# Performance work log

Measured on AMD Instinct MI355X. Metric: run time of the kernel, lower is better.

Reference implementation:

```python
import jax, jax.numpy as jnp
import numpy as np

N, M, E, F, OUT = 20000, 2048, 320000, 512, 2
HID = F // 2
NEG_ATT = 0.2   # leaky_relu slope inside HypergraphConv attention
NEG = 0.01      # default F.leaky_relu / nn.LeakyReLU slope
EPS = 1e-5      # GraphNorm eps


def setup_inputs() -> dict:
    key = jax.random.key(0)
    ks = jax.random.split(key, 12)
    nrm = lambda k, shape, s=0.05: (jax.random.normal(k, shape, jnp.float32) * s)
    row = jax.random.randint(ks[1], (E,), 0, N)
    col = jax.random.randint(ks[2], (E,), 0, M)
    return dict(
        x=nrm(ks[0], (N, F), 1.0),
        edge_index=jnp.stack([row, col]),                 # [2, E] int32
        edge_attr=nrm(ks[3], (M, F), 1.0),
        W1=nrm(ks[4], (F, F)), att1=nrm(ks[5], (2 * F,)), b1=jnp.zeros((F,), jnp.float32),
        W2=nrm(ks[6], (F, F)), att2=nrm(ks[7], (2 * F,)), b2=jnp.zeros((F,), jnp.float32),
        gn1_w=jnp.ones((F,), jnp.float32), gn1_b=jnp.zeros((F,), jnp.float32), gn1_ms=jnp.ones((F,), jnp.float32),
        gn2_w=jnp.ones((F,), jnp.float32), gn2_b=jnp.zeros((F,), jnp.float32), gn2_ms=jnp.ones((F,), jnp.float32),
        fc1_W=nrm(ks[8], (F, HID)), fc1_b=jnp.zeros((HID,), jnp.float32),
        fc2_W=nrm(ks[9], (F, HID)), fc2_b=jnp.zeros((HID,), jnp.float32),
        cls_W=nrm(ks[10], (HID, OUT)), cls_b=jnp.zeros((OUT,), jnp.float32),
    )


def _segsum(v, idx, n):
    return jax.ops.segment_sum(v, idx, num_segments=n)


def hypergraph_conv(x, edge_attr, row, col, W, att, bias):
    """PyG HypergraphConv, heads=1, use_attention=True, attention_mode='node'."""
    xl = x @ W                          # [N, F] node features after lin
    el = edge_attr @ W                  # [M, F] hyperedge features after lin
    # attention logits per incidence: (cat[x_i, e_j] * att).sum(-1)
    pre = xl[row] @ att[:F] + el[col] @ att[F:]           # [E]
    alpha = jax.nn.leaky_relu(pre, NEG_ATT)
    # softmax grouped by hyperedge (col)
    amax = jax.ops.segment_max(alpha, col, num_segments=M)
    amax = jnp.where(jnp.isfinite(amax), amax, 0.0)
    ex = jnp.exp(alpha - amax[col])
    denom = _segsum(ex, col, M)
    alpha = ex / jnp.maximum(denom, 1e-16)[col]           # [E]
    # degree normalizations (hyperedge_weight = 1)
    ones = jnp.ones((row.shape[0],), xl.dtype)
    deg_n = _segsum(ones, row, N)
    Dinv = jnp.where(deg_n > 0, 1.0 / deg_n, 0.0)         # [N]
    deg_e = _segsum(ones, col, M)
    Binv = jnp.where(deg_e > 0, 1.0 / deg_e, 0.0)         # [M]
    # propagate 1: nodes -> hyperedges
    edge_feat = _segsum((alpha * Binv[col])[:, None] * xl[row], col, M)   # [M, F]
    # propagate 2: hyperedges -> nodes
    out = _segsum((alpha * Dinv[row])[:, None] * edge_feat[col], row, N)  # [N, F]
    return out + bias


def graph_norm(x, w, b, ms):
    # single graph (batch=None): normalize over all nodes
    mean = x.mean(axis=0)
    out = x - ms * mean
    var = (out * out).mean(axis=0)
    return out / jnp.sqrt(var + EPS) * w + b


def reference(x, edge_index, edge_attr,
              W1, att1, b1, W2, att2, b2,
              gn1_w, gn1_b, gn1_ms, gn2_w, gn2_b, gn2_ms,
              fc1_W, fc1_b, fc2_W, fc2_b, cls_W, cls_b):
    row, col = edge_index[0], edge_index[1]
    h = hypergraph_conv(x, edge_attr, row, col, W1, att1, b1)
    h = jax.nn.leaky_relu(graph_norm(h, gn1_w, gn1_b, gn1_ms), NEG)
    out = jax.nn.leaky_relu(h @ fc1_W + fc1_b, NEG)
    h = hypergraph_conv(h, edge_attr, row, col, W2, att2, b2)
    h = jax.nn.leaky_relu(graph_norm(h, gn2_w, gn2_b, gn2_ms), NEG)
    out = out + jax.nn.leaky_relu(h @ fc2_W + fc2_b, NEG)
    logits = out @ cls_W + cls_b
    return logits
```

## Files before the change

kernel.cpp:

```cpp
#include <hip/hip_runtime.h>
#include <math.h>

#define FDIM 512
#define HIDDIM 256
#define HB 128
#define SCH 1024
#define LDSK 32

typedef __bf16 bf16x8 __attribute__((ext_vector_type(8)));
typedef float floatx4 __attribute__((ext_vector_type(4)));

__device__ __forceinline__ float lrelu(float x, float s) { return x >= 0.0f ? x : s * x; }

__device__ __forceinline__ float bf2f(unsigned int u) {
  union { float f; unsigned int i; } v; v.i = u << 16; return v.f;
}
__device__ __forceinline__ unsigned short f2bf(float f) {
  union { float f; unsigned int u; } v; v.f = f;
  unsigned int x = v.u;
  return (unsigned short)((x + 0x7fffu + ((x >> 16) & 1u)) >> 16);
}

__device__ __forceinline__ void async_copy16(const unsigned short* g, unsigned short* l) {
  __builtin_amdgcn_global_load_lds((const __attribute__((address_space(1))) unsigned int*)g,
                                   (__attribute__((address_space(3))) unsigned int*)l, 16, 0, 0);
}

__device__ __forceinline__ float waveReduceSum(float v) {
#pragma unroll
  for (int o = 32; o; o >>= 1) v += __shfl_down(v, o, 64);
  return v;
}

__device__ __forceinline__ float blockReduceSum256(float v) {
  __shared__ float sm[4];
  int lane = threadIdx.x & 63, w = threadIdx.x >> 6;
  v = waveReduceSum(v);
  __syncthreads();
  if (lane == 0) sm[w] = v;
  __syncthreads();
  return sm[0] + sm[1] + sm[2] + sm[3];
}

__device__ __forceinline__ float blockReduceMax256(float v) {
  __shared__ float sm[4];
  int lane = threadIdx.x & 63, w = threadIdx.x >> 6;
#pragma unroll
  for (int o = 32; o; o >>= 1) v = fmaxf(v, __shfl_down(v, o, 64));
  __syncthreads();
  if (lane == 0) sm[w] = v;
  __syncthreads();
  return fmaxf(fmaxf(sm[0], sm[1]), fmaxf(sm[2], sm[3]));
}

__global__ __launch_bounds__(256) void k_hist2(const int* __restrict__ row, const int* __restrict__ col,
                                               int* __restrict__ cnt_r, int* __restrict__ cnt_c,
                                               int E, int nchunk) {
  __shared__ int h[2048];
  int b = blockIdx.x, t = threadIdx.x;
  for (int i = t; i < 2048; i += 256) h[i] = 0;
  __syncthreads();
  int s = b * nchunk, e = min(E, s + nchunk);
  for (int j = s + t; j < e; j += 256) {
    atomicAdd(&h[col[j]], 1);
    atomicAdd(&cnt_r[row[j]], 1);
  }
  __syncthreads();
  for (int i = t; i < 2048; i += 256) {
    int v = h[i];
    if (v) atomicAdd(&cnt_c[i], v);
  }
}

__global__ __launch_bounds__(256) void k_scan_part(const int* __restrict__ cnt, int* __restrict__ off,
                                                   int* __restrict__ btot, int n) {
  int b = blockIdx.x, t = threadIdx.x;
  int base = b * SCH + t * 4;
  int v[4];
#pragma unroll
  for (int i = 0; i < 4; ++i) v[i] = (base + i < n) ? cnt[base + i] : 0;
  int s = v[0] + v[1] + v[2] + v[3];
  int lane = t & 63, w = t >> 6;
  int x = s;
#pragma unroll
  for (int o = 1; o < 64; o <<= 1) {
    int y = __shfl_up(x, o, 64);
    if (lane >= o) x += y;
  }
  __shared__ int ws[4];
  if (lane == 63) ws[w] = x;
  __syncthreads();
  int wpre = 0;
  for (int i = 0; i < w; ++i) wpre += ws[i];
  int run = wpre + x - s;
#pragma unroll
  for (int i = 0; i < 4; ++i) {
    if (base + i < n) off[base + i] = run;
    run += v[i];
  }
  if (t == 255) btot[b] = wpre + x;
}

__global__ __launch_bounds__(256) void k_scan_mid(int* __restrict__ btot, int nb) {
  int t = threadIdx.x;
  int v = (t < nb) ? btot[t] : 0;
  int lane = t & 63, w = t >> 6;
  int x = v;
#pragma unroll
  for (int o = 1; o < 64; o <<= 1) {
    int y = __shfl_up(x, o, 64);
    if (lane >= o) x += y;
  }
  __shared__ int ws[4];
  if (lane == 63) ws[w] = x;
  __syncthreads();
  int wpre = 0;
  for (int i = 0; i < w; ++i) wpre += ws[i];
  if (t < nb) btot[t] = wpre + x - v;
  if (t == 255) btot[nb] = wpre + x;
}

__global__ __launch_bounds__(256) void k_scan_add(int* __restrict__ off, const int* __restrict__ btot,
                                                  int n, int nb) {
  int b = blockIdx.x, t = threadIdx.x;
  int base = b * SCH + t * 4;
  int add = btot[b];
#pragma unroll
  for (int i = 0; i < 4; ++i)
    if (base + i < n) off[base + i] += add;
  if (b == 0 && t == 0) off[n] = btot[nb];
}

__global__ __launch_bounds__(256) void k_scan2048(const int* __restrict__ cnt, int* __restrict__ off,
                                                  int* __restrict__ gcur) {
  int t = threadIdx.x;
  int base = t * 8;
  int v[8];
#pragma unroll
  for (int i = 0; i < 8; ++i) v[i] = cnt[base + i];
  int s = 0;
#pragma unroll
  for (int i = 0; i < 8; ++i) s += v[i];
  int lane = t & 63, w = t >> 6;
  int x = s;
#pragma unroll
  for (int o = 1; o < 64; o <<= 1) {
    int y = __shfl_up(x, o, 64);
    if (lane >= o) x += y;
  }
  __shared__ int ws[4];
  if (lane == 63) ws[w] = x;
  __syncthreads();
  int wpre = 0;
  for (int i = 0; i < w; ++i) wpre += ws[i];
  int run = wpre + x - s;
#pragma unroll
  for (int i = 0; i < 8; ++i) {
    off[base + i] = run;
    gcur[base + i] = run;
    run += v[i];
  }
  if (t == 255) off[2048] = wpre + x;
}

__global__ __launch_bounds__(256) void k_fill3(const int* __restrict__ row, const int* __restrict__ col,
                                               int* __restrict__ gcur, const int* __restrict__ off_r,
                                               int* __restrict__ cur_r, int* __restrict__ csr_c,
                                               int* __restrict__ rj, int* __restrict__ cj,
                                               int* __restrict__ pos_r, int E, int nchunk) {
  __shared__ int h[2048];
  __shared__ int lbase[2048];
  int b = blockIdx.x, t = threadIdx.x;
  for (int i = t; i < 2048; i += 256) h[i] = 0;
  __syncthreads();
  int s = b * nchunk, e = min(E, s + nchunk);
  for (int j = s + t; j < e; j += 256) atomicAdd(&h[col[j]], 1);
  __syncthreads();
  for (int i = t; i < 2048; i += 256) {
    int c = h[i];
    lbase[i] = c ? atomicAdd(&gcur[i], c) : 0;
    h[i] = 0;
  }
  __syncthreads();
  for (int j = s + t; j < e; j += 256) {
    int r = row[j], c = col[j];
    int slot_c = lbase[c] + atomicAdd(&h[c], 1);
    csr_c[slot_c] = j;
    rj[slot_c] = r;
    int slot_r = off_r[r] + atomicAdd(&cur_r[r], 1);
    cj[slot_r] = c;
    pos_r[j] = slot_r;
  }
}

__global__ __launch_bounds__(256) void k_hi(const float* __restrict__ A, unsigned short* __restrict__ hi, int n4) {
  int i = blockIdx.x * 256 + threadIdx.x;
  if (i < n4) {
    float4 v = ((const float4*)A)[i];
    ushort4 h;
    h.x = f2bf(v.x); h.y = f2bf(v.y); h.z = f2bf(v.z); h.w = f2bf(v.w);
    ((ushort4*)hi)[i] = h;
  }
}

__global__ __launch_bounds__(256) void k_prep_w_hi(const float* __restrict__ W, unsigned short* __restrict__ th,
                                                   int K, int Nc) {
  int n = blockIdx.x * 16 + (threadIdx.x & 15);
  int k = blockIdx.y * 16 + (threadIdx.x >> 4);
  th[(size_t)n * K + k] = f2bf(W[(size_t)k * Nc + n]);
}

__global__ __launch_bounds__(256) void k_prep_w(const float* __restrict__ W, unsigned short* __restrict__ th,
                                                unsigned short* __restrict__ tl, int K, int Nc) {
  int n = blockIdx.x * 16 + (threadIdx.x & 15);
  int k = blockIdx.y * 16 + (threadIdx.x >> 4);
  float v = W[(size_t)k * Nc + n];
  unsigned short h = f2bf(v);
  unsigned short l = f2bf(v - bf2f(h));
  th[(size_t)n * K + k] = h;
  tl[(size_t)n * K + k] = l;
}

__global__ __launch_bounds__(256) void k_wv(const float* __restrict__ W, const float* __restrict__ att,
                                            float* __restrict__ wv) {
  int lane = threadIdx.x & 63, w = threadIdx.x >> 6;
  int k = blockIdx.x * 4 + w;
  float s = 0.f;
  for (int f = lane; f < FDIM; f += 64) s = fmaf(W[(size_t)k * FDIM + f], att[f], s);
  s = waveReduceSum(s);
  if (lane == 0) wv[k] = s;
}

__global__ __launch_bounds__(256) void k_ea(const float* __restrict__ X, const float* __restrict__ wv,
                                            float* __restrict__ out, int Mr) {
  int lane = threadIdx.x & 63, w = threadIdx.x >> 6;
  int m = blockIdx.x * 4 + w;
  if (m < Mr) {
    float s = 0.f;
    for (int f = lane; f < FDIM; f += 64) s = fmaf(X[(size_t)m * FDIM + f], wv[f], s);
    s = waveReduceSum(s);
    if (lane == 0) out[m] = s;
  }
}

__global__ __launch_bounds__(256, 1) void gemm_conv(const unsigned short* __restrict__ Ah,
                                                    const unsigned short* __restrict__ Bth,
                                                    unsigned short* __restrict__ Cb,
                                                    const float* __restrict__ att, float* __restrict__ xa,
                                                    int Mr, int K, int Nc) {
  __shared__ unsigned short lds[2 * 128 * LDSK];
  int tid = threadIdx.x, lane = tid & 63, w = tid >> 6;
  int wr = w >> 1, wc = w & 1;
  int rowB = blockIdx.y * 128, colB = blockIdx.x * 128;

  const unsigned short* src = (w < 2) ? Ah : Bth;
  int baseRow = ((w < 2) ? rowB : colB) + 64 * (w & 1);
  int maxRow = (w < 2) ? (Mr - 1) : (Nc - 1);
  int slr = lane >> 2, slc = lane & 3;
  unsigned short* dstBase = &lds[((w >> 1) * 128 + (w & 1) * 64) * LDSK];

  size_t gro[4];
#pragma unroll
  for (int seg = 0; seg < 4; ++seg) {
    int rg = baseRow + seg * 16 + slr;
    if (rg > maxRow) rg = maxRow;
    gro[seg] = (size_t)rg * K + slc * 8;
  }

  floatx4 zero4 = {0.f, 0.f, 0.f, 0.f};
  floatx4 acc[4][4];
#pragma unroll
  for (int i = 0; i < 4; ++i)
#pragma unroll
    for (int j = 0; j < 4; ++j) acc[i][j] = zero4;

  int fr = lane & 15, fq = lane >> 4;
  int offA = (wr * 64 + fr) * LDSK + fq * 8;
  int offB = 128 * LDSK + (wc * 64 + fr) * LDSK + fq * 8;

  for (int k0 = 0; k0 < K; k0 += 32) {
#pragma unroll
    for (int seg = 0; seg < 4; ++seg) async_copy16(src + gro[seg] + k0, dstBase + seg * 16 * LDSK);
    __syncthreads();
    bf16x8 a[4], b[4];
#pragma unroll
    for (int t = 0; t < 4; ++t) {
      a[t] = *(const bf16x8*)(&lds[offA + t * 16 * LDSK]);
      b[t] = *(const bf16x8*)(&lds[offB + t * 16 * LDSK]);
    }
#pragma unroll
    for (int ti = 0; ti < 4; ++ti)
#pragma unroll
      for (int tj = 0; tj < 4; ++tj)
        acc[ti][tj] = __builtin_amdgcn_mfma_f32_16x16x32_bf16(a[ti], b[tj], acc[ti][tj], 0, 0, 0);
    __syncthreads();
  }

  int colL = colB + wc * 64 + fr;
  int rowL = rowB + wr * 64 + fq * 4;
  float attv[4];
#pragma unroll
  for (int tj = 0; tj < 4; ++tj) attv[tj] = att[colL + tj * 16];
#pragma unroll
  for (int ti = 0; ti < 4; ++ti) {
#pragma unroll
    for (int r = 0; r < 4; ++r) {
      int rr = rowL + ti * 16 + r;
      if (rr < Mr) {
        float dot = 0.f;
#pragma unroll
        for (int tj = 0; tj < 4; ++tj) {
          float v = acc[ti][tj][r];
          Cb[(size_t)rr * Nc + colL + tj * 16] = f2bf(v);
          dot = fmaf(v, attv[tj], dot);
        }
#pragma unroll
        for (int o = 1; o < 16; o <<= 1) dot += __shfl_xor(dot, o, 64);
        if ((lane & 15) == 0) atomicAdd(&xa[rr], dot);
      }
    }
  }
}

template <int EPI>
__global__ __launch_bounds__(256, 1) void gemm_fc(const unsigned short* __restrict__ Ahi,
                                                  const unsigned short* __restrict__ Bthi,
                                                  const unsigned short* __restrict__ Btlo,
                                                  float* __restrict__ Cf, const float* __restrict__ bias,
                                                  int Mr, int K, int Nc) {
  __shared__ unsigned short lds[3 * 128 * LDSK];
  int tid = threadIdx.x, lane = tid & 63, w = tid >> 6;
  int wr = w >> 1, wc = w & 1;
  int rowB = blockIdx.y * 128, colB = blockIdx.x * 128;

  const unsigned short* src;
  int baseRow, maxRow, nseg;
  unsigned short* dstBase;
  if (w < 2) { src = Ahi; baseRow = rowB + 64 * w; maxRow = Mr - 1; nseg = 4; dstBase = &lds[w * 64 * LDSK]; }
  else if (w == 2) { src = Bthi; baseRow = colB; maxRow = Nc - 1; nseg = 8; dstBase = &lds[128 * LDSK]; }
  else { src = Btlo; baseRow = colB; maxRow = Nc - 1; nseg = 8; dstBase = &lds[2 * 128 * LDSK]; }

  int slr = lane >> 2, slc = lane & 3;
  size_t gro[8];
  for (int seg = 0; seg < nseg; ++seg) {
    int rg = baseRow + seg * 16 + slr;
    if (rg > maxRow) rg = maxRow;
    gro[seg] = (size_t)rg * K + slc * 8;
  }

  floatx4 zero4 = {0.f, 0.f, 0.f, 0.f};
  floatx4 acc[4][4];
#pragma unroll
  for (int i = 0; i < 4; ++i)
#pragma unroll
    for (int j = 0; j < 4; ++j) acc[i][j] = zero4;

  int fr = lane & 15, fq = lane >> 4;
  int offA = (wr * 64 + fr) * LDSK + fq * 8;
  int offBh = 128 * LDSK + (wc * 64 + fr) * LDSK + fq * 8;

  for (int k0 = 0; k0 < K; k0 += 32) {
    for (int seg = 0; seg < nseg; ++seg) async_copy16(src + gro[seg] + k0, dstBase + seg * 16 * LDSK);
    __syncthreads();
    bf16x8 a[4], bh[4], bl[4];
#pragma unroll
    for (int t = 0; t < 4; ++t) {
      a[t] = *(const bf16x8*)(&lds[offA + t * 16 * LDSK]);
      bh[t] = *(const bf16x8*)(&lds[offBh + t * 16 * LDSK]);
      bl[t] = *(const bf16x8*)(&lds[128 * LDSK + offBh + t * 16 * LDSK]);
    }
#pragma unroll
    for (int ti = 0; ti < 4; ++ti)
#pragma unroll
      for (int tj = 0; tj < 4; ++tj) {
        acc[ti][tj] = __builtin_amdgcn_mfma_f32_16x16x32_bf16(a[ti], bh[tj], acc[ti][tj], 0, 0, 0);
        acc[ti][tj] = __builtin_amdgcn_mfma_f32_16x16x32_bf16(a[ti], bl[tj], acc[ti][tj], 0, 0, 0);
      }
    __syncthreads();
  }

  int colL = colB + wc * 64 + fr;
  int rowL = rowB + wr * 64 + fq * 4;
#pragma unroll
  for (int tj = 0; tj < 4; ++tj) {
    int c = colL + tj * 16;
    float bb = bias[c];
#pragma unroll
    for (int ti = 0; ti < 4; ++ti) {
#pragma unroll
      for (int r = 0; r < 4; ++r) {
        int rr = rowL + ti * 16 + r;
        if (rr < Mr) {
          float v = lrelu(acc[ti][tj][r] + bb, 0.01f);
          if (EPI == 1) Cf[(size_t)rr * Nc + c] = v;
          else Cf[(size_t)rr * Nc + c] += v;
        }
      }
    }
  }
}

__global__ __launch_bounds__(256) void k_attn(const float* __restrict__ xa, const float* __restrict__ ea,
                                              const int* __restrict__ rj, const int* __restrict__ csr_c,
                                              const int* __restrict__ pos_r, const int* __restrict__ off_c,
                                              float* __restrict__ aj, float* __restrict__ arj) {
  int m = blockIdx.x;
  int s = off_c[m], e_ = off_c[m + 1];
  float eam = ea[m];
  int t = threadIdx.x;
  float mx = -3.402823466e38f;
  for (int j = s + t; j < e_; j += 256) {
    float a = lrelu(xa[rj[j]] + eam, 0.2f);
    aj[j] = a;
    mx = fmaxf(mx, a);
  }
  mx = blockReduceMax256(mx);
  float sum = 0.f;
  for (int j = s + t; j < e_; j += 256) sum += expf(aj[j] - mx);
  sum = blockReduceSum256(sum);
  float inv = 1.0f / fmaxf(sum, 1e-16f);
  for (int j = s + t; j < e_; j += 256) {
    float a = expf(aj[j] - mx) * inv;
    aj[j] = a;
    arj[pos_r[csr_c[j]]] = a;
  }
}

__global__ __launch_bounds__(256) void k_prop_col(const unsigned short* __restrict__ xl,
                                                  const float* __restrict__ aj, const int* __restrict__ rj,
                                                  const int* __restrict__ off_c, unsigned short* __restrict__ ef) {
  int m = blockIdx.x;
  int s = off_c[m], e_ = off_c[m + 1];
  int cnt = e_ - s;
  __shared__ int sidx[512];
  __shared__ float swgt[512];
  __shared__ float pf[4][512];
  int t = threadIdx.x, lane = t & 63, w = t >> 6;
  float acc[8] = {0, 0, 0, 0, 0, 0, 0, 0};
  for (int base = 0; base < cnt; base += 512) {
    int n = min(512, cnt - base);
    for (int j = t; j < n; j += 256) {
      sidx[j] = rj[s + base + j];
      swgt[j] = aj[s + base + j];
    }
    __syncthreads();
    int j = w;
    for (; j + 8 <= n; j += 8) {
      int r0 = sidx[j], r1 = sidx[j + 4];
      float w0 = swgt[j], w1 = swgt[j + 4];
      bf16x8 v0 = *(const bf16x8*)(xl + (size_t)r0 * FDIM + lane * 8);
      bf16x8 v1 = *(const bf16x8*)(xl + (size_t)r1 * FDIM + lane * 8);
#pragma unroll
      for (int i = 0; i < 8; ++i) acc[i] = fmaf(w0, (float)v0[i], acc[i]);
#pragma unroll
      for (int i = 0; i < 8; ++i) acc[i] = fmaf(w1, (float)v1[i], acc[i]);
    }
    for (; j < n; j += 4) {
      int r = sidx[j];
      float wt = swgt[j];
      bf16x8 v = *(const bf16x8*)(xl + (size_t)r * FDIM + lane * 8);
#pragma unroll
      for (int i = 0; i < 8; ++i) acc[i] = fmaf(wt, (float)v[i], acc[i]);
    }
    __syncthreads();
  }
  float binv = cnt > 0 ? 1.0f / (float)cnt : 0.0f;
#pragma unroll
  for (int i = 0; i < 8; i += 2) *(float2*)&pf[w][lane * 8 + i] = make_float2(acc[i] * binv, acc[i + 1] * binv);
  __syncthreads();
  float2 r0 = ((const float2*)pf[0])[t], r1 = ((const float2*)pf[1])[t];
  float2 r2 = ((const float2*)pf[2])[t], r3 = ((const float2*)pf[3])[t];
  float a0 = r0.x + r1.x + r2.x + r3.x;
  float a1 = r0.y + r1.y + r2.y + r3.y;
  unsigned int o = (unsigned int)f2bf(a0) | ((unsigned int)f2bf(a1) << 16);
  ((unsigned int*)(ef + (size_t)m * FDIM))[t] = o;
}

__global__ __launch_bounds__(256) void k_prop_row(const unsigned short* __restrict__ ef,
                                                  const float* __restrict__ arj, const int* __restrict__ cj,
                                                  const int* __restrict__ off_r, const float* __restrict__ bias,
                                                  unsigned short* __restrict__ hb) {
  int nB = blockIdx.x;
  int s = off_r[nB], e_ = off_r[nB + 1];
  int cnt = e_ - s;
  __shared__ int sidx[512];
  __shared__ float swgt[512];
  __shared__ float pf[4][512];
  int t = threadIdx.x, lane = t & 63, w = t >> 6;
  float acc[8] = {0, 0, 0, 0, 0, 0, 0, 0};
  for (int base = 0; base < cnt; base += 512) {
    int n = min(512, cnt - base);
    for (int j = t; j < n; j += 256) {
      sidx[j] = cj[s + base + j];
      swgt[j] = arj[s + base + j];
    }
    __syncthreads();
    int j = w;
    for (; j + 8 <= n; j += 8) {
      int r0 = sidx[j], r1 = sidx[j + 4];
      float w0 = swgt[j], w1 = swgt[j + 4];
      bf16x8 v0 = *(const bf16x8*)(ef + (size_t)r0 * FDIM + lane * 8);
      bf16x8 v1 = *(const bf16x8*)(ef + (size_t)r1 * FDIM + lane * 8);
#pragma unroll
      for (int i = 0; i < 8; ++i) acc[i] = fmaf(w0, (float)v0[i], acc[i]);
#pragma unroll
      for (int i = 0; i < 8; ++i) acc[i] = fmaf(w1, (float)v1[i], acc[i]);
    }
    for (; j < n; j += 4) {
      int r = sidx[j];
      float wt = swgt[j];
      bf16x8 v = *(const bf16x8*)(ef + (size_t)r * FDIM + lane * 8);
#pragma unroll
      for (int i = 0; i < 8; ++i) acc[i] = fmaf(wt, (float)v[i], acc[i]);
    }
    __syncthreads();
  }
  float dinv = cnt > 0 ? 1.0f / (float)cnt : 0.0f;
#pragma unroll
  for (int i = 0; i < 8; i += 2) *(float2*)&pf[w][lane * 8 + i] = make_float2(acc[i] * dinv, acc[i + 1] * dinv);
  __syncthreads();
  float2 r0 = ((const float2*)pf[0])[t], r1 = ((const float2*)pf[1])[t];
  float2 r2 = ((const float2*)pf[2])[t], r3 = ((const float2*)pf[3])[t];
  float a0 = r0.x + r1.x + r2.x + r3.x + bias[2 * t];
  float a1 = r0.y + r1.y + r2.y + r3.y + bias[2 * t + 1];
  unsigned int o = (unsigned int)f2bf(a0) | ((unsigned int)f2bf(a1) << 16);
  ((unsigned int*)(hb + (size_t)nB * FDIM))[t] = o;
}

__global__ __launch_bounds__(256) void k_stats(const unsigned short* __restrict__ hb, float* __restrict__ gsum,
                                               float* __restrict__ gsq, int N) {
  int t = threadIdx.x;
  float s0 = 0, q0 = 0, s1 = 0, q1 = 0;
  for (int r = blockIdx.x; r < N; r += gridDim.x) {
    unsigned int u = ((const unsigned int*)(hb + (size_t)r * FDIM))[t];
    float v0 = bf2f(u & 0xffffu), v1 = bf2f(u >> 16);
    s0 += v0; q0 = fmaf(v0, v0, q0);
    s1 += v1; q1 = fmaf(v1, v1, q1);
  }
  atomicAdd(&gsum[2 * t], s0);
  atomicAdd(&gsq[2 * t], q0);
  atomicAdd(&gsum[2 * t + 1], s1);
  atomicAdd(&gsq[2 * t + 1], q1);
}

__global__ __launch_bounds__(512) void k_nparam(const float* __restrict__ gsum, const float* __restrict__ gsq,
                                                const float* __restrict__ ms, const float* __restrict__ w,
                                                float* __restrict__ msm, float* __restrict__ scl, float invn) {
  int f = threadIdx.x;
  float mean = gsum[f] * invn;
  float ex2 = gsq[f] * invn;
  float m = ms[f];
  float var = ex2 - (2.0f * m - m * m) * mean * mean;
  scl[f] = w[f] / sqrtf(var + 1e-5f);
  msm[f] = m * mean;
}

__global__ __launch_bounds__(256) void k_napply(const unsigned short* __restrict__ hb,
                                                const float* __restrict__ msm, const float* __restrict__ scl,
                                                const float* __restrict__ b, unsigned short* __restrict__ hi,
                                                int total2) {
  int i = blockIdx.x * 256 + threadIdx.x;
  if (i < total2) {
    int f2 = i & 255;
    unsigned int u = ((const unsigned int*)hb)[i];
    float v0 = bf2f(u & 0xffffu), v1 = bf2f(u >> 16);
    int f0 = 2 * f2, f1 = 2 * f2 + 1;
    v0 = lrelu((v0 - msm[f0]) * scl[f0] + b[f0], 0.01f);
    v1 = lrelu((v1 - msm[f1]) * scl[f1] + b[f1], 0.01f);
    ((unsigned int*)hi)[i] = (unsigned int)f2bf(v0) | ((unsigned int)f2bf(v1) << 16);
  }
}

__global__ __launch_bounds__(256) void k_cls(const float* __restrict__ out1, const float* __restrict__ W,
                                             const float* __restrict__ b, float* __restrict__ logits, int N) {
  __shared__ float Ws[512];
  int t = threadIdx.x;
  Ws[t] = W[t];
  Ws[256 + t] = W[256 + t];
  __syncthreads();
  int lane = t & 63, w = t >> 6;
  int r = blockIdx.x * 4 + w;
  if (r < N) {
    float a0 = 0.f, a1 = 0.f;
    for (int k = lane; k < 256; k += 64) {
      float v = out1[(size_t)r * 256 + k];
      a0 = fmaf(v, Ws[2 * k], a0);
      a1 = fmaf(v, Ws[2 * k + 1], a1);
    }
#pragma unroll
    for (int o = 32; o; o >>= 1) {
      a0 += __shfl_down(a0, o, 64);
      a1 += __shfl_down(a1, o, 64);
    }
    if (lane == 0) {
      logits[(size_t)r * 2] = a0 + b[0];
      logits[(size_t)r * 2 + 1] = a1 + b[1];
    }
  }
}

extern "C" void kernel_launch(void* const* d_in, const int* in_sizes, int n_in,
                              void* d_out, int out_size, void* d_ws, size_t ws_size,
                              hipStream_t stream) {
  const float* x      = (const float*)d_in[0];
  const int*   eidx   = (const int*)d_in[1];
  const float* eattr  = (const float*)d_in[2];
  const float* W1     = (const float*)d_in[3];
  const float* att1   = (const float*)d_in[4];
  const float* b1     = (const float*)d_in[5];
  const float* W2     = (const float*)d_in[6];
  const float* att2   = (const float*)d_in[7];
  const float* b2     = (const float*)d_in[8];
  const float* gn1_w  = (const float*)d_in[9];
  const float* gn1_b  = (const float*)d_in[10];
  const float* gn1_ms = (const float*)d_in[11];
  const float* gn2_w  = (const float*)d_in[12];
  const float* gn2_b  = (const float*)d_in[13];
  const float* gn2_ms = (const float*)d_in[14];
  const float* fc1_W  = (const float*)d_in[15];
  const float* fc1_b  = (const float*)d_in[16];
  const float* fc2_W  = (const float*)d_in[17];
  const float* fc2_b  = (const float*)d_in[18];
  const float* cls_W  = (const float*)d_in[19];
  const float* cls_b  = (const float*)d_in[20];
  float* logits = (float*)d_out;

  const int N = in_sizes[0] / FDIM;
  const int E = in_sizes[1] / 2;
  const int M = in_sizes[2] / FDIM;
  const int* row = eidx;
  const int* col = eidx + E;
  const size_t NS = (size_t)N * FDIM;
  const size_t MS = (size_t)M * FDIM;

  char* base = (char*)d_ws;
  auto alloc = [&](size_t bytes) { char* r = base; base += (bytes + 255) & ~(size_t)255; return r; };

  unsigned short* xhi = (unsigned short*)alloc(NS * 2);
  unsigned short* xl  = (unsigned short*)alloc(NS * 2);
  unsigned short* hb  = (unsigned short*)alloc(NS * 2);
  unsigned short* ef  = (unsigned short*)alloc(MS * 2);
  float* out1 = (float*)alloc((size_t)N * HIDDIM * 4);
  unsigned short* w1th = (unsigned short*)alloc(FDIM * FDIM * 2);
  unsigned short* w2th = (unsigned short*)alloc(FDIM * FDIM * 2);
  unsigned short* f1th = (unsigned short*)alloc(FDIM * HIDDIM * 2);
  unsigned short* f1tl = (unsigned short*)alloc(FDIM * HIDDIM * 2);
  unsigned short* f2th = (unsigned short*)alloc(FDIM * HIDDIM * 2);
  unsigned short* f2tl = (unsigned short*)alloc(FDIM * HIDDIM * 2);
  float* wv1 = (float*)alloc(FDIM * 4);
  float* wv2 = (float*)alloc(FDIM * 4);
  float* xa = (float*)alloc((size_t)N * 4);
  float* ea1 = (float*)alloc((size_t)M * 4);
  float* ea2 = (float*)alloc((size_t)M * 4);
  float* aj  = (float*)alloc((size_t)E * 4);
  float* arj = (float*)alloc((size_t)E * 4);
  float* gsum = (float*)alloc(FDIM * 4);
  float* gsq  = (float*)alloc(FDIM * 4);
  float* msm  = (float*)alloc(FDIM * 4);
  float* scl  = (float*)alloc(FDIM * 4);
  int* cnt_r = (int*)alloc((size_t)(2 * N + M) * 4);
  int* cur_r = cnt_r + N;
  int* cnt_c = cur_r + N;
  int* off_r = (int*)alloc((size_t)(N + 1) * 4);
  int* off_c = (int*)alloc((size_t)(M + 1) * 4);
  int* gcur  = (int*)alloc((size_t)M * 4);
  int* csr_c = (int*)alloc((size_t)E * 4);
  int* rj    = (int*)alloc((size_t)E * 4);
  int* cj    = (int*)alloc((size_t)E * 4);
  int* pos_r = (int*)alloc((size_t)E * 4);
  int* btot  = (int*)alloc(512 * 4);

  hipMemsetAsync(cnt_r, 0, sizeof(int) * (size_t)(2 * N + M), stream);

  int nchunk = (E + HB - 1) / HB;
  int nbR = (N + SCH - 1) / SCH;
  k_hist2<<<HB, 256, 0, stream>>>(row, col, cnt_r, cnt_c, E, nchunk);
  k_scan_part<<<nbR, 256, 0, stream>>>(cnt_r, off_r, btot, N);
  k_scan_mid<<<1, 256, 0, stream>>>(btot, nbR);
  k_scan_add<<<nbR, 256, 0, stream>>>(off_r, btot, N, nbR);
  k_scan2048<<<1, 256, 0, stream>>>(cnt_c, off_c, gcur);
  k_fill3<<<HB, 256, 0, stream>>>(row, col, gcur, off_r, cur_r, csr_c, rj, cj, pos_r, E, nchunk);

  k_hi<<<(int)((NS / 4 + 255) / 256), 256, 0, stream>>>(x, xhi, (int)(NS / 4));
  k_prep_w_hi<<<dim3(FDIM / 16, FDIM / 16), 256, 0, stream>>>(W1, w1th, FDIM, FDIM);
  k_prep_w_hi<<<dim3(FDIM / 16, FDIM / 16), 256, 0, stream>>>(W2, w2th, FDIM, FDIM);
  k_prep_w<<<dim3(HIDDIM / 16, FDIM / 16), 256, 0, stream>>>(fc1_W, f1th, f1tl, FDIM, HIDDIM);
  k_prep_w<<<dim3(HIDDIM / 16, FDIM / 16), 256, 0, stream>>>(fc2_W, f2th, f2tl, FDIM, HIDDIM);
  k_wv<<<FDIM / 4, 256, 0, stream>>>(W1, att1 + FDIM, wv1);
  k_wv<<<FDIM / 4, 256, 0, stream>>>(W2, att2 + FDIM, wv2);
  k_ea<<<(M + 3) / 4, 256, 0, stream>>>(eattr, wv1, ea1, M);
  k_ea<<<(M + 3) / 4, 256, 0, stream>>>(eattr, wv2, ea2, M);

  int gN128 = (N + 127) / 128;
  int napply_grid = (int)((NS / 2 + 255) / 256);

  hipMemsetAsync(xa, 0, (size_t)N * 4, stream);
  gemm_conv<<<dim3(FDIM / 128, gN128), 256, 0, stream>>>(xhi, w1th, xl, att1, xa, N, FDIM, FDIM);
  k_attn<<<M, 256, 0, stream>>>(xa, ea1, rj, csr_c, pos_r, off_c, aj, arj);
  k_prop_col<<<M, 256, 0, stream>>>(xl, aj, rj, off_c, ef);
  k_prop_row<<<N, 256, 0, stream>>>(ef, arj, cj, off_r, b1, hb);
  hipMemsetAsync(gsum, 0, sizeof(float) * 2 * FDIM, stream);
  k_stats<<<256, 256, 0, stream>>>(hb, gsum, gsq, N);
  k_nparam<<<1, 512, 0, stream>>>(gsum, gsq, gn1_ms, gn1_w, msm, scl, 1.0f / (float)N);
  k_napply<<<napply_grid, 256, 0, stream>>>(hb, msm, scl, gn1_b, xhi, (int)(NS / 2));
  gemm_fc<1><<<dim3(HIDDIM / 128, gN128), 256, 0, stream>>>(xhi, f1th, f1tl, out1, fc1_b, N, FDIM, HIDDIM);

  hipMemsetAsync(xa, 0, (size_t)N * 4, stream);
  gemm_conv<<<dim3(FDIM / 128, gN128), 256, 0, stream>>>(xhi, w2th, xl, att2, xa, N, FDIM, FDIM);
  k_attn<<<M, 256, 0, stream>>>(xa, ea2, rj, csr_c, pos_r, off_c, aj, arj);
  k_prop_col<<<M, 256, 0, stream>>>(xl, aj, rj, off_c, ef);
  k_prop_row<<<N, 256, 0, stream>>>(ef, arj, cj, off_r, b2, hb);
  hipMemsetAsync(gsum, 0, sizeof(float) * 2 * FDIM, stream);
  k_stats<<<256, 256, 0, stream>>>(hb, gsum, gsq, N);
  k_nparam<<<1, 512, 0, stream>>>(gsum, gsq, gn2_ms, gn2_w, msm, scl, 1.0f / (float)N);
  k_napply<<<napply_grid, 256, 0, stream>>>(hb, msm, scl, gn2_b, xhi, (int)(NS / 2));
  gemm_fc<2><<<dim3(HIDDIM / 128, gN128), 256, 0, stream>>>(xhi, f2th, f2tl, out1, fc2_b, N, FDIM, HIDDIM);

  k_cls<<<(N + 3) / 4, 256, 0, stream>>>(out1, cls_W, cls_b, logits, N);
}
```

Before: 598.2 us.

## Sort hyperedge segments by row, fuse attention prep kernels, unroll column gather

Adds a per-hyperedge bitonic sort of the column-CSR entries by node index, so gathers from xl in the column propagation walk memory in ascending row order. The per-layer wv and edge-attention dot kernels are merged into single launches that handle both layers, cutting launch count and re-reads of edge_attr. The column propagation loop is unrolled to keep four row loads in flight instead of two. The sort adds an extra kernel over every hyperedge, and segments longer than 512 entries are left unsorted.

```diff
diff --git a/kernel.cpp b/kernel.cpp
--- a/kernel.cpp
+++ b/kernel.cpp
@@ -193,6 +193,44 @@
   }
 }
 
+__global__ __launch_bounds__(256) void k_sortseg(int* __restrict__ rj, int* __restrict__ csr_c,
+                                                 const int* __restrict__ off_c) {
+  int m = blockIdx.x;
+  int s = off_c[m], e = off_c[m + 1];
+  int n = e - s;
+  if (n > 512) return;
+  __shared__ int key[512];
+  __shared__ int val[512];
+  int t = threadIdx.x;
+  for (int i = t; i < 512; i += 256) {
+    if (i < n) { key[i] = rj[s + i]; val[i] = csr_c[s + i]; }
+    else { key[i] = 0x7fffffff; val[i] = 0; }
+  }
+  __syncthreads();
+  for (int k = 2; k <= 512; k <<= 1) {
+    for (int j = k >> 1; j > 0; j >>= 1) {
+#pragma unroll
+      for (int p = 0; p < 2; ++p) {
+        int i = t + p * 256;
+        int ixj = i ^ j;
+        if (ixj > i) {
+          bool up = ((i & k) == 0);
+          int a = key[i], b = key[ixj];
+          if ((a > b) == up) {
+            key[i] = b; key[ixj] = a;
+            int va = val[i]; val[i] = val[ixj]; val[ixj] = va;
+          }
+        }
+      }
+      __syncthreads();
+    }
+  }
+  for (int i = t; i < n; i += 256) {
+    rj[s + i] = key[i];
+    csr_c[s + i] = val[i];
+  }
+}
+
 __global__ __launch_bounds__(256) void k_hi(const float* __restrict__ A, unsigned short* __restrict__ hi, int n4) {
   int i = blockIdx.x * 256 + threadIdx.x;
   if (i < n4) {
@@ -221,25 +259,35 @@
   tl[(size_t)n * K + k] = l;
 }
 
-__global__ __launch_bounds__(256) void k_wv(const float* __restrict__ W, const float* __restrict__ att,
-                                            float* __restrict__ wv) {
+__global__ __launch_bounds__(256) void k_wv2(const float* __restrict__ W1, const float* __restrict__ a1,
+                                             const float* __restrict__ W2, const float* __restrict__ a2,
+                                             float* __restrict__ wv1, float* __restrict__ wv2) {
   int lane = threadIdx.x & 63, w = threadIdx.x >> 6;
   int k = blockIdx.x * 4 + w;
+  const float* W = blockIdx.y ? W2 : W1;
+  const float* a = blockIdx.y ? a2 : a1;
+  float* wv = blockIdx.y ? wv2 : wv1;
   float s = 0.f;
-  for (int f = lane; f < FDIM; f += 64) s = fmaf(W[(size_t)k * FDIM + f], att[f], s);
+  for (int f = lane; f < FDIM; f += 64) s = fmaf(W[(size_t)k * FDIM + f], a[f], s);
   s = waveReduceSum(s);
   if (lane == 0) wv[k] = s;
 }
 
-__global__ __launch_bounds__(256) void k_ea(const float* __restrict__ X, const float* __restrict__ wv,
-                                            float* __restrict__ out, int Mr) {
+__global__ __launch_bounds__(256) void k_ea2(const float* __restrict__ X, const float* __restrict__ wv1,
+                                             const float* __restrict__ wv2, float* __restrict__ ea1,
+                                             float* __restrict__ ea2, int Mr) {
   int lane = threadIdx.x & 63, w = threadIdx.x >> 6;
   int m = blockIdx.x * 4 + w;
   if (m < Mr) {
-    float s = 0.f;
-    for (int f = lane; f < FDIM; f += 64) s = fmaf(X[(size_t)m * FDIM + f], wv[f], s);
-    s = waveReduceSum(s);
-    if (lane == 0) out[m] = s;
+    float s1 = 0.f, s2 = 0.f;
+    for (int f = lane; f < FDIM; f += 64) {
+      float v = X[(size_t)m * FDIM + f];
+      s1 = fmaf(v, wv1[f], s1);
+      s2 = fmaf(v, wv2[f], s2);
+    }
+    s1 = waveReduceSum(s1);
+    s2 = waveReduceSum(s2);
+    if (lane == 0) { ea1[m] = s1; ea2[m] = s2; }
   }
 }
 
@@ -445,15 +493,21 @@
     }
     __syncthreads();
     int j = w;
-    for (; j + 8 <= n; j += 8) {
-      int r0 = sidx[j], r1 = sidx[j + 4];
-      float w0 = swgt[j], w1 = swgt[j + 4];
+    for (; j + 16 <= n; j += 16) {
+      int r0 = sidx[j], r1 = sidx[j + 4], r2 = sidx[j + 8], r3 = sidx[j + 12];
+      float w0 = swgt[j], w1 = swgt[j + 4], w2 = swgt[j + 8], w3 = swgt[j + 12];
       bf16x8 v0 = *(const bf16x8*)(xl + (size_t)r0 * FDIM + lane * 8);
       bf16x8 v1 = *(const bf16x8*)(xl + (size_t)r1 * FDIM + lane * 8);
+      bf16x8 v2 = *(const bf16x8*)(xl + (size_t)r2 * FDIM + lane * 8);
+      bf16x8 v3 = *(const bf16x8*)(xl + (size_t)r3 * FDIM + lane * 8);
 #pragma unroll
       for (int i = 0; i < 8; ++i) acc[i] = fmaf(w0, (float)v0[i], acc[i]);
 #pragma unroll
       for (int i = 0; i < 8; ++i) acc[i] = fmaf(w1, (float)v1[i], acc[i]);
+#pragma unroll
+      for (int i = 0; i < 8; ++i) acc[i] = fmaf(w2, (float)v2[i], acc[i]);
+#pragma unroll
+      for (int i = 0; i < 8; ++i) acc[i] = fmaf(w3, (float)v3[i], acc[i]);
     }
     for (; j < n; j += 4) {
       int r = sidx[j];
@@ -680,16 +734,15 @@
   k_scan_add<<<nbR, 256, 0, stream>>>(off_r, btot, N, nbR);
   k_scan2048<<<1, 256, 0, stream>>>(cnt_c, off_c, gcur);
   k_fill3<<<HB, 256, 0, stream>>>(row, col, gcur, off_r, cur_r, csr_c, rj, cj, pos_r, E, nchunk);
+  k_sortseg<<<M, 256, 0, stream>>>(rj, csr_c, off_c);
 
   k_hi<<<(int)((NS / 4 + 255) / 256), 256, 0, stream>>>(x, xhi, (int)(NS / 4));
   k_prep_w_hi<<<dim3(FDIM / 16, FDIM / 16), 256, 0, stream>>>(W1, w1th, FDIM, FDIM);
   k_prep_w_hi<<<dim3(FDIM / 16, FDIM / 16), 256, 0, stream>>>(W2, w2th, FDIM, FDIM);
   k_prep_w<<<dim3(HIDDIM / 16, FDIM / 16), 256, 0, stream>>>(fc1_W, f1th, f1tl, FDIM, HIDDIM);
   k_prep_w<<<dim3(HIDDIM / 16, FDIM / 16), 256, 0, stream>>>(fc2_W, f2th, f2tl, FDIM, HIDDIM);
-  k_wv<<<FDIM / 4, 256, 0, stream>>>(W1, att1 + FDIM, wv1);
-  k_wv<<<FDIM / 4, 256, 0, stream>>>(W2, att2 + FDIM, wv2);
-  k_ea<<<(M + 3) / 4, 256, 0, stream>>>(eattr, wv1, ea1, M);
-  k_ea<<<(M + 3) / 4, 256, 0, stream>>>(eattr, wv2, ea2, M);
+  k_wv2<<<dim3(FDIM / 4, 2), 256, 0, stream>>>(W1, att1 + FDIM, W2, att2 + FDIM, wv1, wv2);
+  k_ea2<<<(M + 3) / 4, 256, 0, stream>>>(eattr, wv1, wv2, ea1, ea2, M);
 
   int gN128 = (N + 127) / 128;
   int napply_grid = (int)((NS / 2 + 255) / 256);
```

After: 601.8 us. Within noise of the previous version (+0.6%).
